# Kernel tuning notes

Hardware: AMD Instinct MI355X
Metric: run time of the kernel (lower is better)

The kernel has to match this reference:

```python
import jax, jax.numpy as jnp
import numpy as np

B, R, D, N, E = 1024, 512, 64, 100000, 2000000


def setup_inputs() -> dict:
    key = jax.random.key(0)
    ks = jax.random.split(key, 12)
    rel_embs = jax.random.normal(ks[0], (B, R, D), dtype=jnp.float32)
    query_rels = jax.random.randint(ks[1], (B,), 0, R)
    query_entities = jax.random.randint(ks[2], (B,), 0, N)
    edge_index = jax.random.randint(ks[3], (2, E), 0, N)
    edge_type = jax.random.randint(ks[4], (E,), 0, R)
    s = 0.05
    W1 = jax.random.normal(ks[5], (2 * D + 4, D), jnp.float32) * s
    b1 = jnp.zeros((D,), jnp.float32)
    W2 = jax.random.normal(ks[6], (D, D // 2), jnp.float32) * s
    b2 = jnp.zeros((D // 2,), jnp.float32)
    W3 = jax.random.normal(ks[7], (D // 2, D // 4), jnp.float32) * s
    b3 = jnp.zeros((D // 4,), jnp.float32)
    # original init: last layer weight = 0, bias = 0.85
    W4 = jnp.zeros((D // 4, 1), jnp.float32)
    b4 = jnp.full((1,), 0.85, jnp.float32)
    return {
        "relation_embeddings": rel_embs,
        "query_rels": query_rels,
        "query_entities": query_entities,
        "edge_index": edge_index,
        "edge_type": edge_type,
        "num_nodes": N,
        "num_relations": R,
        "W1": W1, "b1": b1, "W2": W2, "b2": b2,
        "W3": W3, "b3": b3, "W4": W4, "b4": b4,
    }


def reference(relation_embeddings, query_rels, query_entities, edge_index,
              edge_type, num_nodes, num_relations, W1, b1, W2, b2, W3, b3, W4, b4):
    Bq, Rr, Dd = relation_embeddings.shape
    Ee = edge_type.shape[0]
    dt = relation_embeddings.dtype
    src, dst = edge_index[0], edge_index[1]

    # per-node, per-relation incident-edge counts (self-loop counted once, matching OR mask)
    counts = jnp.zeros((num_nodes, num_relations), dt)
    counts = counts.at[src, edge_type].add(jnp.ones((Ee,), dt))
    counts = counts.at[dst, edge_type].add(jnp.where(src != dst, 1.0, 0.0).astype(dt))
    deg = counts.sum(axis=-1)                    # [N]

    cnt_q = counts[query_entities]               # [B, R]
    deg_q = deg[query_entities]                  # [B]

    # query relation embedding (zero if index out of range)
    valid_rel = (query_rels < Rr)
    rel_emb = relation_embeddings[jnp.arange(Bq), jnp.clip(query_rels, 0, Rr - 1)]
    rel_emb = jnp.where(valid_rel[:, None], rel_emb, 0.0)

    # mean embedding of relations on edges incident to the query entity
    num = jnp.einsum('br,brd->bd', cnt_q, relation_embeddings)
    entity_emb = jnp.where(deg_q[:, None] > 0, num / jnp.maximum(deg_q, 1.0)[:, None], 0.0)
    valid_ent = (query_entities < num_nodes)
    entity_emb = jnp.where(valid_ent[:, None], entity_emb, 0.0)

    # graph statistics (constants w.r.t. gradients, as in the torch code)
    rel_count = jnp.zeros((num_relations,), dt).at[edge_type].add(jnp.ones((Ee,), dt))
    fE = jnp.asarray(max(Ee, 1), dt)
    rel_freq = jnp.minimum(jnp.where(valid_rel, rel_count[jnp.clip(query_rels, 0, num_relations - 1)], 0.0) / fE, 1.0)
    ent_deg_norm = jnp.minimum(jnp.where(valid_ent, deg_q, 0.0) / fE, 1.0)
    density = jnp.full((Bq,), min(Ee / max(num_nodes * num_nodes, 1), 1.0), dt)
    stats = jax.lax.stop_gradient(jnp.stack([rel_freq, ent_deg_norm, rel_freq, density], axis=-1))

    feat = jnp.concatenate([rel_emb, entity_emb, stats], axis=-1)   # [B, 2D+4]
    h = jax.nn.relu(feat @ W1 + b1)
    h = jax.nn.relu(h @ W2 + b2)
    h = jax.nn.relu(h @ W3 + b3)
    gate = jax.nn.sigmoid(h @ W4 + b4)[:, 0]                         # [B]
    return gate
```

## Files before the change

### kernel.cpp

```cpp
#include <hip/hip_runtime.h>
#include <math.h>


#define HSZ   4096
#define HMASK (HSZ - 1)
#define NBLK_SCATTER 2048
#define RMAX 512
#define EMPTY_SLOT 0xFFFFFFFFu

__device__ __forceinline__ unsigned hash_u(unsigned x) {
    x *= 2654435761u;
    x ^= x >> 15;
    return x & HMASK;
}

__global__ void k_insert(const int* __restrict__ qent,
                         const int* __restrict__ num_nodes,
                         unsigned* __restrict__ table, int B) {
    int b = blockIdx.x * blockDim.x + threadIdx.x;
    if (b >= B) return;
    int ent = qent[b];
    if (ent < 0 || ent >= *num_nodes) return;
    unsigned packed = ((unsigned)ent << 12) | (unsigned)b;
    unsigned h = hash_u((unsigned)ent);
    while (true) {
        unsigned old = atomicCAS(&table[h], EMPTY_SLOT, packed);
        if (old == EMPTY_SLOT) break;
        h = (h + 1) & HMASK;
    }
}

__device__ __forceinline__ void probe_add(unsigned node, int t,
                                          const unsigned* __restrict__ table,
                                          float* __restrict__ cnt_q, int R) {
    unsigned h = hash_u(node);
    while (true) {
        unsigned slot = table[h];
        if (slot == EMPTY_SLOT) return;
        if ((slot >> 12) == node)
            atomicAdd(&cnt_q[(size_t)(slot & 0xFFFu) * R + t], 1.0f);
        h = (h + 1) & HMASK;
    }
}

__global__ __launch_bounds__(256) void k_scatter(
    const int* __restrict__ edge_index, const int* __restrict__ edge_type,
    const unsigned* __restrict__ table, float* __restrict__ cnt_q,
    int* __restrict__ rel_count_i, int E, int R) {
    __shared__ int hist[RMAX];
    for (int i = threadIdx.x; i < RMAX; i += blockDim.x) hist[i] = 0;
    __syncthreads();

    const int* srcp = edge_index;
    const int* dstp = edge_index + E;
    int tid = blockIdx.x * blockDim.x + threadIdx.x;
    int stride = gridDim.x * blockDim.x;

    int E4 = E >> 2;
    for (int e4 = tid; e4 < E4; e4 += stride) {
        int4 s4 = ((const int4*)srcp)[e4];
        int4 d4 = ((const int4*)dstp)[e4];
        int4 t4 = ((const int4*)edge_type)[e4];
        int ss[4] = {s4.x, s4.y, s4.z, s4.w};
        int dd[4] = {d4.x, d4.y, d4.z, d4.w};
        int tt[4] = {t4.x, t4.y, t4.z, t4.w};
#pragma unroll
        for (int j = 0; j < 4; ++j) {
            int t = tt[j];
            if ((unsigned)t < (unsigned)RMAX) atomicAdd(&hist[t], 1);
            probe_add((unsigned)ss[j], t, table, cnt_q, R);
            if (dd[j] != ss[j]) probe_add((unsigned)dd[j], t, table, cnt_q, R);
        }
    }
    for (int e = (E4 << 2) + tid; e < E; e += stride) {
        int s = srcp[e], d = dstp[e], t = edge_type[e];
        if ((unsigned)t < (unsigned)RMAX) atomicAdd(&hist[t], 1);
        probe_add((unsigned)s, t, table, cnt_q, R);
        if (d != s) probe_add((unsigned)d, t, table, cnt_q, R);
    }

    __syncthreads();
    for (int i = threadIdx.x; i < R; i += blockDim.x) {
        int v = hist[i];
        if (v) atomicAdd(&rel_count_i[i], v);
    }
}

__global__ __launch_bounds__(256) void k_final(
    const float* __restrict__ emb,
    const int* __restrict__ qrel, const int* __restrict__ qent,
    const int* __restrict__ num_nodes_p, const int* __restrict__ num_rel_p,
    const float* __restrict__ cnt_q, const int* __restrict__ rel_count_i,
    const float* __restrict__ W1, const float* __restrict__ b1,
    const float* __restrict__ W2, const float* __restrict__ b2,
    const float* __restrict__ W3, const float* __restrict__ b3,
    const float* __restrict__ W4, const float* __restrict__ b4,
    float* __restrict__ out, int R, float fE, float fEcnt) {
    const int D = 64;
    int b = blockIdx.x;
    int tid = threadIdx.x;
    int wave = tid >> 6;
    int lane = tid & 63;

    __shared__ float s_cnt[RMAX];
    __shared__ float s_acc[4 * 64];
    __shared__ float s_feat[132];
    __shared__ float s_h1[64];
    __shared__ float s_h2[32];
    __shared__ float s_h3[16];
    __shared__ float s_red[256];

    float dpart = 0.f;
    for (int r = tid; r < R; r += 256) {
        float c = cnt_q[(size_t)b * R + r];
        s_cnt[r] = c;
        dpart += c;
    }
    s_red[tid] = dpart;
    __syncthreads();
    for (int off = 128; off > 0; off >>= 1) {
        if (tid < off) s_red[tid] += s_red[tid + off];
        __syncthreads();
    }
    float deg = s_red[0];

    const float* embB = emb + (size_t)b * R * D;
    float acc = 0.f;
    int rchunk = R >> 2;
    int r0 = wave * rchunk, r1 = r0 + rchunk;
    for (int r = r0; r < r1; ++r) {
        float c = s_cnt[r];
        if (c != 0.0f) acc += c * embB[(size_t)r * D + lane];
    }
    s_acc[wave * 64 + lane] = acc;
    __syncthreads();

    int qr = qrel[b];
    bool valid_rel = (qr >= 0) && (qr < R);
    int qrc = qr < 0 ? 0 : (qr > R - 1 ? R - 1 : qr);
    int N = *num_nodes_p;
    bool valid_ent = ((unsigned)qent[b] < (unsigned)N);

    if (tid < 64) {
        float num = s_acc[tid] + s_acc[64 + tid] + s_acc[128 + tid] + s_acc[192 + tid];
        float ent_emb = (deg > 0.f) ? num / fmaxf(deg, 1.f) : 0.f;
        if (!valid_ent) ent_emb = 0.f;
        float re = valid_rel ? embB[(size_t)qrc * D + tid] : 0.f;
        s_feat[tid] = re;
        s_feat[64 + tid] = ent_emb;
    }
    if (tid == 0) {
        int nr = *num_rel_p;
        int qrc2 = qr < 0 ? 0 : (qr > nr - 1 ? nr - 1 : qr);
        float rc = valid_rel ? (float)rel_count_i[qrc2] : 0.f;
        float rel_freq = fminf(rc / fE, 1.f);
        float dq = valid_ent ? deg : 0.f;
        float edn = fminf(dq / fE, 1.f);
        double nn = (double)N * (double)N;
        float density = (float)fmin((double)fEcnt / fmax(nn, 1.0), 1.0);
        s_feat[128] = rel_freq;
        s_feat[129] = edn;
        s_feat[130] = rel_freq;
        s_feat[131] = density;
    }
    __syncthreads();

    if (tid < 64) {
        float s = b1[tid];
#pragma unroll 4
        for (int k = 0; k < 132; ++k) s += s_feat[k] * W1[k * 64 + tid];
        s_h1[tid] = fmaxf(s, 0.f);
    }
    __syncthreads();
    if (tid < 32) {
        float s = b2[tid];
#pragma unroll 4
        for (int k = 0; k < 64; ++k) s += s_h1[k] * W2[k * 32 + tid];
        s_h2[tid] = fmaxf(s, 0.f);
    }
    __syncthreads();
    if (tid < 16) {
        float s = b3[tid];
#pragma unroll 4
        for (int k = 0; k < 32; ++k) s += s_h2[k] * W3[k * 16 + tid];
        s_h3[tid] = fmaxf(s, 0.f);
    }
    __syncthreads();
    if (tid == 0) {
        float s = b4[0];
#pragma unroll
        for (int k = 0; k < 16; ++k) s += s_h3[k] * W4[k];
        out[b] = 1.f / (1.f + expf(-s));
    }
}

extern "C" void kernel_launch(void* const* d_in, const int* in_sizes, int n_in,
                              void* d_out, int out_size, void* d_ws, size_t ws_size,
                              hipStream_t stream) {
    const float* emb   = (const float*)d_in[0];
    const int*   qrel  = (const int*)d_in[1];
    const int*   qent  = (const int*)d_in[2];
    const int*   eidx  = (const int*)d_in[3];
    const int*   etyp  = (const int*)d_in[4];
    const int*   nn    = (const int*)d_in[5];
    const int*   nr    = (const int*)d_in[6];
    const float* W1    = (const float*)d_in[7];
    const float* b1    = (const float*)d_in[8];
    const float* W2    = (const float*)d_in[9];
    const float* b2    = (const float*)d_in[10];
    const float* W3    = (const float*)d_in[11];
    const float* b3    = (const float*)d_in[12];
    const float* W4    = (const float*)d_in[13];
    const float* b4    = (const float*)d_in[14];
    float* out = (float*)d_out;

    int B = in_sizes[1];
    int E = in_sizes[4];
    int R = in_sizes[0] / (B * 64);

    char* ws = (char*)d_ws;
    float* cnt_q       = (float*)ws;
    int*   rel_count_i = (int*)(ws + (size_t)B * R * 4);
    unsigned* table    = (unsigned*)(rel_count_i + R);

    hipMemsetAsync(cnt_q, 0, (size_t)(B * R + R) * 4, stream);
    hipMemsetAsync(table, 0xFF, HSZ * 4, stream);

    k_insert<<<(B + 255) / 256, 256, 0, stream>>>(qent, nn, table, B);
    k_scatter<<<NBLK_SCATTER, 256, 0, stream>>>(eidx, etyp, table, cnt_q,
                                                rel_count_i, E, R);
    float fE = (float)(E > 1 ? E : 1);
    k_final<<<B, 256, 0, stream>>>(emb, qrel, qent, nn, nr, cnt_q, rel_count_i,
                                   W1, b1, W2, b2, W3, b3, W4, b4, out,
                                   R, fE, (float)E);
}
```

Baseline: 96.14 us.

## Fuse workspace zeroing and hash insert; compact nonzero counts before embedding gather

Two memsets and the insert kernel are replaced by a single setup kernel. It zeroes cnt_q with float4 stores, clears rel_count, and has one block build the hash table, which removes launch overhead. The final kernel now loads its counts row with float4 and builds a ballot-compacted list of nonzero relations, so the four waves spread the weighted embedding sum over only those nonzeros. The count load and the setup kernel hardcode R<=1024, R divisible by 4, and B*R small enough for 512 blocks, and the single-block hash insert is serial over B.

```diff
diff --git a/kernel.cpp b/kernel.cpp
--- a/kernel.cpp
+++ b/kernel.cpp
@@ -14,19 +14,31 @@
     return x & HMASK;
 }
 
-__global__ void k_insert(const int* __restrict__ qent,
-                         const int* __restrict__ num_nodes,
-                         unsigned* __restrict__ table, int B) {
-    int b = blockIdx.x * blockDim.x + threadIdx.x;
-    if (b >= B) return;
-    int ent = qent[b];
-    if (ent < 0 || ent >= *num_nodes) return;
-    unsigned packed = ((unsigned)ent << 12) | (unsigned)b;
-    unsigned h = hash_u((unsigned)ent);
-    while (true) {
-        unsigned old = atomicCAS(&table[h], EMPTY_SLOT, packed);
-        if (old == EMPTY_SLOT) break;
-        h = (h + 1) & HMASK;
+__global__ __launch_bounds__(256) void k_setup(
+    const int* __restrict__ qent, const int* __restrict__ num_nodes,
+    float4* __restrict__ cnt_q4, int* __restrict__ rel_count_i,
+    unsigned* __restrict__ table, int nBR4, int R, int B) {
+    int bx = blockIdx.x, tid = threadIdx.x;
+    if (bx < 512) {
+        int i = bx * 256 + tid;
+        if (i < nBR4) cnt_q4[i] = make_float4(0.f, 0.f, 0.f, 0.f);
+    } else if (bx == 512) {
+        for (int i = tid; i < R; i += 256) rel_count_i[i] = 0;
+    } else {
+        for (int i = tid; i < HSZ; i += 256) table[i] = EMPTY_SLOT;
+        __syncthreads();
+        int N = *num_nodes;
+        for (int b = tid; b < B; b += 256) {
+            int ent = qent[b];
+            if (ent < 0 || ent >= N) continue;
+            unsigned packed = ((unsigned)ent << 12) | (unsigned)b;
+            unsigned h = hash_u((unsigned)ent);
+            while (true) {
+                unsigned old = atomicCAS(&table[h], EMPTY_SLOT, packed);
+                if (old == EMPTY_SLOT) break;
+                h = (h + 1) & HMASK;
+            }
+        }
     }
 }
 
@@ -103,6 +115,9 @@
     int lane = tid & 63;
 
     __shared__ float s_cnt[RMAX];
+    __shared__ int   s_idx[RMAX];
+    __shared__ float s_c[RMAX];
+    __shared__ int   s_n;
     __shared__ float s_acc[4 * 64];
     __shared__ float s_feat[132];
     __shared__ float s_h1[64];
@@ -111,10 +126,14 @@
     __shared__ float s_red[256];
 
     float dpart = 0.f;
-    for (int r = tid; r < R; r += 256) {
-        float c = cnt_q[(size_t)b * R + r];
-        s_cnt[r] = c;
-        dpart += c;
+    {
+        const float4* row4 = (const float4*)(cnt_q + (size_t)b * R);
+        int n4 = R >> 2;
+        if (tid < n4) {
+            float4 v = row4[tid];
+            ((float4*)s_cnt)[tid] = v;
+            dpart = v.x + v.y + v.z + v.w;
+        }
     }
     s_red[tid] = dpart;
     __syncthreads();
@@ -124,14 +143,28 @@
     }
     float deg = s_red[0];
 
+    if (wave == 0) {
+        int base = 0;
+        for (int c8 = 0; c8 < 8; ++c8) {
+            int r = c8 * 64 + lane;
+            float c = s_cnt[r];
+            unsigned long long m = __ballot(c != 0.f);
+            if (c != 0.f) {
+                int pos = base + __popcll(m & ((1ull << lane) - 1ull));
+                s_idx[pos] = r;
+                s_c[pos] = c;
+            }
+            base += __popcll(m);
+        }
+        if (lane == 0) s_n = base;
+    }
+    __syncthreads();
+
     const float* embB = emb + (size_t)b * R * D;
+    int nnz = s_n;
     float acc = 0.f;
-    int rchunk = R >> 2;
-    int r0 = wave * rchunk, r1 = r0 + rchunk;
-    for (int r = r0; r < r1; ++r) {
-        float c = s_cnt[r];
-        if (c != 0.0f) acc += c * embB[(size_t)r * D + lane];
-    }
+    for (int i = wave; i < nnz; i += 4)
+        acc += s_c[i] * embB[(size_t)s_idx[i] * D + lane];
     s_acc[wave * 64 + lane] = acc;
     __syncthreads();
 
@@ -223,10 +256,9 @@
     int*   rel_count_i = (int*)(ws + (size_t)B * R * 4);
     unsigned* table    = (unsigned*)(rel_count_i + R);
 
-    hipMemsetAsync(cnt_q, 0, (size_t)(B * R + R) * 4, stream);
-    hipMemsetAsync(table, 0xFF, HSZ * 4, stream);
-
-    k_insert<<<(B + 255) / 256, 256, 0, stream>>>(qent, nn, table, B);
+    int nBR4 = (B * R) >> 2;
+    k_setup<<<514, 256, 0, stream>>>(qent, nn, (float4*)cnt_q, rel_count_i,
+                                     table, nBR4, R, B);
     k_scatter<<<NBLK_SCATTER, 256, 0, stream>>>(eidx, etyp, table, cnt_q,
                                                 rel_count_i, E, R);
     float fE = (float)(E > 1 ? E : 1);
```

Measured after the change: 86.92 us. 1.11x faster.
